# Kernel tuning notes

Measured on AMD Instinct MI355X. Metric: run time of the kernel, lower is better.

## Reference

```python
import jax, jax.numpy as jnp
from jax import lax
import numpy as np

EPS = 1e-5  # torch BatchNorm2d default eps


def _conv_bn_relu_pool(x, w, b, g, beta):
    # Conv2d(k=3, pad=1) -> BatchNorm2d (training mode: batch stats, biased var)
    # -> ReLU -> MaxPool2d(2). x: (N, Cin, H, W), w: (Cout, Cin, 3, 3)
    y = lax.conv_general_dilated(x, w, window_strides=(1, 1), padding='SAME',
                                 dimension_numbers=('NCHW', 'OIHW', 'NCHW'))
    y = y + b[None, :, None, None]
    m = y.mean(axis=(0, 2, 3), keepdims=True)
    v = y.var(axis=(0, 2, 3), keepdims=True)  # biased, matches torch normalization
    y = (y - m) * lax.rsqrt(v + EPS)
    y = y * g[None, :, None, None] + beta[None, :, None, None]
    y = jax.nn.relu(y)
    return lax.reduce_window(y, -jnp.inf, lax.max, (1, 1, 2, 2), (1, 1, 2, 2), 'VALID')


def setup_inputs() -> dict:
    key = jax.random.key(0)
    ks = jax.random.split(key, 20)
    B, T, C, H, W = 16, 64, 3, 32, 32
    F_in = 64 * (H // 4) * (W // 4)  # 4096 flattened CNN features per frame
    n = lambda i, shape, s=0.05: jax.random.normal(ks[i], shape, jnp.float32) * s
    return {
        'x_1': jax.random.normal(ks[0], (B, T, C, H, W), jnp.float32),
        'x_2': jax.random.normal(ks[1], (B, T, C, H, W), jnp.float32),
        'conv1_w': n(2, (64, 2 * C, 3, 3)), 'conv1_b': n(3, (64,)),
        'bn1_g': 1.0 + n(4, (64,)), 'bn1_b': n(5, (64,)),
        'conv2_w': n(6, (64, 64, 3, 3)), 'conv2_b': n(7, (64,)),
        'bn2_g': 1.0 + n(8, (64,)), 'bn2_b': n(9, (64,)),
        'R_w': n(10, (100, 400)), 'R_b': n(11, (100,)),
        'Q_w': n(12, (100, F_in + 100)), 'Q_b': n(13, (100,)),
        'O_w': n(14, (128, 400)), 'O_b': n(15, (128,)),
        'fc1_w': n(16, (64, 128)), 'fc1_b': n(17, (64,)),
        'fc2_w': n(18, (1, 64)), 'fc2_b': n(19, (1,)),
    }


def reference(x_1, x_2, conv1_w, conv1_b, bn1_g, bn1_b, conv2_w, conv2_b,
              bn2_g, bn2_b, R_w, R_b, Q_w, Q_b, O_w, O_b,
              fc1_w, fc1_b, fc2_w, fc2_b):
    B, T = x_1.shape[0], x_1.shape[1]
    x = jnp.concatenate([x_1, x_2], axis=2)            # (B, T, 2C, H, W)
    xr = x.reshape((B * T,) + x.shape[2:])             # fold time into batch
    y = _conv_bn_relu_pool(xr, conv1_w, conv1_b, bn1_g, bn1_b)
    y = _conv_bn_relu_pool(y, conv2_w, conv2_b, bn2_g, bn2_b)
    feats = y.reshape(B, T, -1)                        # (B, T, 4096)

    A = jnp.array([0.0, 0.25, 0.5, 0.95], jnp.float32)  # leaky-integrator decays
    Q_SIZE = 100

    def step(Ha, in_t):
        # Ha: (B, 4, 100); in_t: (B, F_in)
        Hf = Ha.reshape(B, -1)                          # (B, 400) = H_Size
        Rt = jnp.tanh(Hf @ R_w.T + R_b)                 # (B, 100)
        Qt = jnp.tanh(jnp.concatenate([in_t, Rt], axis=1) @ Q_w.T + Q_b)  # (B,100)
        Ha_new = A[None, :, None] * Ha + (1.0 - A)[None, :, None] * Qt[:, None, :]
        return Ha_new, None

    Ha0 = jnp.zeros((B, len(A), Q_SIZE), jnp.float32)
    Ha_T, _ = lax.scan(step, Ha0, jnp.swapaxes(feats, 0, 1))  # scan over T

    # only the last-timestep RNN output feeds the head (out[:, -1, :])
    out_last = jnp.tanh(Ha_T.reshape(B, -1) @ O_w.T + O_b)    # (B, 128)
    h = jax.nn.relu(out_last @ fc1_w.T + fc1_b)               # (B, 64)
    return jax.nn.sigmoid(h @ fc2_w.T + fc2_b)                # (B, 1)
```

## Files before the change

### kernel.cpp

```cpp
#include <hip/hip_runtime.h>
#include <math.h>


typedef __attribute__((ext_vector_type(8))) short s8v;
typedef __attribute__((ext_vector_type(4))) float f32x4;

__device__ __forceinline__ unsigned short f2bf(float f) {
  union { float f; unsigned u; } x; x.f = f;
  return (unsigned short)((x.u + 0x7FFFu + ((x.u >> 16) & 1u)) >> 16);
}
__device__ __forceinline__ float bf2f(unsigned short u) {
  union { unsigned u; float f; } x; x.u = ((unsigned)u) << 16; return x.f;
}
__device__ __forceinline__ float ftanh(float x) {
  float e = __expf(2.f * x);
  return 1.f - 2.f * __builtin_amdgcn_rcpf(e + 1.f);
}

__global__ __launch_bounds__(256)
void w1_pack(const float* __restrict__ w1, unsigned short* __restrict__ wB1)
{
  int i = blockIdx.x*256 + threadIdx.x;
  if (i < 6144) {
    int kh = i >> 11, rem = i & 2047, co = rem >> 5, k2 = rem & 31;
    unsigned short v = 0;
    if (k2 < 18) {
      int kw = k2 / 6, ci = k2 - 6*kw;
      v = f2bf(w1[co*54 + ci*9 + kh*3 + kw]);
    }
    wB1[i] = v;
  }
}

__global__ __launch_bounds__(256, 4)
void conv1_mfma(const float* __restrict__ x1, const float* __restrict__ x2,
                const unsigned short* __restrict__ wB1,
                float* __restrict__ part,
                unsigned short* __restrict__ pmax1, unsigned short* __restrict__ pmin1)
{
  __shared__ unsigned xin[3688];
  __shared__ float wred[4][4][16][2];
  const int n = blockIdx.x, tid = threadIdx.x;
  const int w = tid >> 6, lane = tid & 63;
  const int q = lane >> 4, r = lane & 15;

  s8v bf[3][4];
  #pragma unroll
  for (int kh = 0; kh < 3; ++kh)
    #pragma unroll
    for (int t = 0; t < 4; ++t)
      bf[kh][t] = *(const s8v*)&wB1[kh*2048 + (((t<<4)+r)<<5) + (q<<3)];

  #pragma unroll
  for (int k = 0; k < 15; ++k) {
    int i = tid + (k<<8);
    if (i < 3688) xin[i] = 0;
  }
  __syncthreads();
  #pragma unroll
  for (int k = 0; k < 12; ++k) {
    int i = tid + (k<<8);
    int cp = i >> 10, p = i & 1023;
    int y = p >> 5, x = p & 31;
    float lo, hi;
    if (cp == 0)      { lo = x1[n*3072 + p];        hi = x1[n*3072 + 1024 + p]; }
    else if (cp == 1) { lo = x1[n*3072 + 2048 + p]; hi = x2[n*3072 + p];        }
    else              { lo = x2[n*3072 + 1024 + p]; hi = x2[n*3072 + 2048 + p]; }
    xin[(y+1)*108 + (x+1)*3 + cp] = (unsigned)f2bf(lo) | ((unsigned)f2bf(hi) << 16);
  }
  __syncthreads();

  float st[4], sq[4];
  #pragma unroll
  for (int t = 0; t < 4; ++t) { st[t] = 0.f; sq[t] = 0.f; }
  float pmx[4][2], pmn[4][2];

  #pragma unroll 1
  for (int xb = 0; xb < 2; ++xb) {
    const int xbase = xb << 4;
    #pragma unroll 2
    for (int j = 0; j < 8; ++j) {
      const int y = (w << 3) + j;
      f32x4 acc[4];
      #pragma unroll
      for (int t = 0; t < 4; ++t) acc[t] = (f32x4){0.f,0.f,0.f,0.f};
      #pragma unroll
      for (int kh = 0; kh < 3; ++kh) {
        int dw = (y + kh)*108 + 3*(xbase + r) + (q << 2);
        union { unsigned u[4]; s8v v; } af;
        af.u[0] = xin[dw];   af.u[1] = xin[dw+1];
        af.u[2] = xin[dw+2]; af.u[3] = xin[dw+3];
        #pragma unroll
        for (int t = 0; t < 4; ++t)
          acc[t] = __builtin_amdgcn_mfma_f32_16x16x32_bf16(af.v, bf[kh][t], acc[t], 0, 0, 0);
      }
      #pragma unroll
      for (int t = 0; t < 4; ++t) {
        st[t] += acc[t][0]+acc[t][1]+acc[t][2]+acc[t][3];
        sq[t] = fmaf(acc[t][0],acc[t][0], fmaf(acc[t][1],acc[t][1],
                fmaf(acc[t][2],acc[t][2], fmaf(acc[t][3],acc[t][3], sq[t]))));
      }
      if ((j & 1) == 0) {
        #pragma unroll
        for (int t = 0; t < 4; ++t) {
          pmx[t][0] = fmaxf(acc[t][0], acc[t][1]); pmx[t][1] = fmaxf(acc[t][2], acc[t][3]);
          pmn[t][0] = fminf(acc[t][0], acc[t][1]); pmn[t][1] = fminf(acc[t][2], acc[t][3]);
        }
      } else {
        const int py = y >> 1;
        #pragma unroll
        for (int t = 0; t < 4; ++t) {
          int co = (t << 4) + r;
          #pragma unroll
          for (int pp = 0; pp < 2; ++pp) {
            float mx = fmaxf(pmx[t][pp], fmaxf(acc[t][2*pp], acc[t][2*pp+1]));
            float mn = fminf(pmn[t][pp], fminf(acc[t][2*pp], acc[t][2*pp+1]));
            int pxp = (xb << 3) + (q << 1) + pp;
            int o = (((n << 8) + (py << 4) + pxp) << 6) + co;
            pmax1[o] = f2bf(mx);
            pmin1[o] = f2bf(mn);
          }
        }
      }
    }
  }

  #pragma unroll
  for (int t = 0; t < 4; ++t) {
    float s = st[t], ss = sq[t];
    s  += __shfl_xor(s, 16);  s  += __shfl_xor(s, 32);
    ss += __shfl_xor(ss, 16); ss += __shfl_xor(ss, 32);
    if (q == 0) { wred[w][t][r][0] = s; wred[w][t][r][1] = ss; }
  }
  __syncthreads();
  if (tid < 64) {
    float s = 0.f, ss = 0.f;
    #pragma unroll
    for (int wv = 0; wv < 4; ++wv) {
      s  += wred[wv][tid >> 4][tid & 15][0];
      ss += wred[wv][tid >> 4][tid & 15][1];
    }
    part[tid*2048 + n*2]     = s;
    part[tid*2048 + n*2 + 1] = ss;
  }
}

__global__ __launch_bounds__(256)
void bn_finalize(const float* __restrict__ part, const float* __restrict__ g,
                 const float* __restrict__ beta, float inv_cnt, float* __restrict__ bn)
{
  __shared__ float red[8];
  const int c = blockIdx.x, tid = threadIdx.x;
  float s = 0.f, ss = 0.f;
  for (int n = tid; n < 1024; n += 256) {
    s  += part[c*2048 + n*2];
    ss += part[c*2048 + n*2 + 1];
  }
  #pragma unroll
  for (int d = 32; d; d >>= 1) { s += __shfl_xor(s, d); ss += __shfl_xor(ss, d); }
  if ((tid & 63) == 0) { red[(tid>>6)*2] = s; red[(tid>>6)*2+1] = ss; }
  __syncthreads();
  if (tid == 0) {
    float S  = red[0]+red[2]+red[4]+red[6];
    float SS = red[1]+red[3]+red[5]+red[7];
    float m  = S * inv_cnt;
    float var = SS * inv_cnt - m*m;
    float sc = g[c] * rsqrtf(var + 1e-5f);
    bn[c]    = sc;
    bn[64+c] = beta[c] - m*sc;
  }
}

__global__ __launch_bounds__(256)
void w2_pack(const float* __restrict__ w2, unsigned short* __restrict__ wB)
{
  int i = blockIdx.x*256 + threadIdx.x;
  if (i < 36864) {
    int khw = i >> 12, rem = i & 4095, co = rem >> 6, ci = rem & 63;
    int chunk = (ci >> 3) ^ (co & 7);
    wB[khw*4096 + co*64 + chunk*8 + (ci & 7)] = f2bf(w2[co*576 + ci*9 + khw]);
  }
}

__global__ __launch_bounds__(256)
void qw_pack(const float* __restrict__ Qw, unsigned short* __restrict__ qB)
{
  int i = blockIdx.x*256 + threadIdx.x;
  if (i < 458752) {
    int j = i >> 12, k = i & 4095;
    qB[i] = (j < 100) ? f2bf(Qw[j*4196 + k]) : (unsigned short)0;
  }
}

__global__ __launch_bounds__(256)
void conv2_mfma(const unsigned short* __restrict__ pmax1,
                const unsigned short* __restrict__ pmin1,
                const float* __restrict__ bn1,
                const unsigned short* __restrict__ wB,
                float* __restrict__ part,
                unsigned short* __restrict__ pmax2, unsigned short* __restrict__ pmin2)
{
  __shared__ unsigned short xin[324*64];
  __shared__ unsigned short wL[9*64*64];
  __shared__ float wred[4][4][16][2];
  __shared__ float bnL[128];
  const int n = blockIdx.x, tid = threadIdx.x;
  const int w = tid >> 6, lane = tid & 63;
  const int q = lane >> 4, col = lane & 15;

  if (tid < 128) bnL[tid] = bn1[tid];
  {
    const s8v* src = (const s8v*)wB;
    s8v* dst = (s8v*)wL;
    #pragma unroll
    for (int i = 0; i < 18; ++i) dst[tid + (i<<8)] = src[tid + (i<<8)];
  }
  __syncthreads();
  {
    #pragma unroll
    for (int k = 0; k < 11; ++k) {
      int i = tid + (k<<8);
      if (i < 324*8) {
        int L = i >> 3, s = i & 7;
        int y = L / 18, x = L - y*18;
        s8v v = (s8v){0,0,0,0,0,0,0,0};
        if (y >= 1 && y <= 16 && x >= 1 && x <= 16) {
          int idx = (((n<<8) + ((y-1)<<4) + (x-1))<<6) + (s<<3);
          s8v mx = *(const s8v*)&pmax1[idx];
          s8v mn = *(const s8v*)&pmin1[idx];
          #pragma unroll
          for (int e = 0; e < 8; ++e) {
            int ci = (s<<3) + e;
            float sc = bnL[ci], sh = bnL[64+ci];
            float vv = bf2f((unsigned short)(sc >= 0.f ? mx[e] : mn[e]));
            v[e] = (short)f2bf(fmaxf(fmaf(vv, sc, sh), 0.f));
          }
        }
        *(s8v*)((char*)xin + L*128 + (((s ^ (L & 7)) << 4))) = v;
      }
    }
  }
  __syncthreads();

  f32x4 acc[4][4];
  #pragma unroll
  for (int mt = 0; mt < 4; ++mt)
    #pragma unroll
    for (int t = 0; t < 4; ++t)
      acc[mt][t] = (f32x4){0.f,0.f,0.f,0.f};

  const int py0 = w << 2;
  #pragma unroll 1
  for (int khw = 0; khw < 9; ++khw) {
    const int kh = khw / 3, kw = khw - 3*kh;
    const char* wslice = (const char*)wL + khw*8192;
    #pragma unroll
    for (int ks = 0; ks < 2; ++ks) {
      const int chunk = (ks << 2) + q;
      s8v bfrag[4];
      #pragma unroll
      for (int t = 0; t < 4; ++t) {
        int co = (t << 4) + col;
        bfrag[t] = *(const s8v*)(wslice + co*128 + (((chunk ^ (co & 7)) << 4)));
      }
      #pragma unroll
      for (int mt = 0; mt < 4; ++mt) {
        int L = (py0 + mt + kh)*18 + (col + kw);
        s8v afrag = *(const s8v*)((const char*)xin + L*128 + (((chunk ^ (L & 7)) << 4)));
        #pragma unroll
        for (int t = 0; t < 4; ++t)
          acc[mt][t] = __builtin_amdgcn_mfma_f32_16x16x32_bf16(afrag, bfrag[t], acc[mt][t], 0, 0, 0);
      }
    }
  }

  #pragma unroll
  for (int t = 0; t < 4; ++t) {
    float s = 0.f, ss = 0.f;
    #pragma unroll
    for (int mt = 0; mt < 4; ++mt)
      #pragma unroll
      for (int r = 0; r < 4; ++r) {
        float v = acc[mt][t][r];
        s += v; ss = fmaf(v, v, ss);
      }
    s  += __shfl_xor(s, 16);  s  += __shfl_xor(s, 32);
    ss += __shfl_xor(ss, 16); ss += __shfl_xor(ss, 32);
    if (q == 0) { wred[w][t][col][0] = s; wred[w][t][col][1] = ss; }
  }
  __syncthreads();
  if (tid < 64) {
    float s = 0.f, ss = 0.f;
    #pragma unroll
    for (int wv = 0; wv < 4; ++wv) {
      s  += wred[wv][tid >> 4][tid & 15][0];
      ss += wred[wv][tid >> 4][tid & 15][1];
    }
    part[tid*2048 + n*2]     = s;
    part[tid*2048 + n*2 + 1] = ss;
  }

  #pragma unroll
  for (int t = 0; t < 4; ++t) {
    int co = (t << 4) + col;
    #pragma unroll
    for (int mp = 0; mp < 2; ++mp) {
      f32x4 a0 = acc[2*mp][t], a1 = acc[2*mp+1][t];
      float mx0 = fmaxf(fmaxf(a0[0], a0[1]), fmaxf(a1[0], a1[1]));
      float mx1 = fmaxf(fmaxf(a0[2], a0[3]), fmaxf(a1[2], a1[3]));
      float mn0 = fminf(fminf(a0[0], a0[1]), fminf(a1[0], a1[1]));
      float mn1 = fminf(fminf(a0[2], a0[3]), fminf(a1[2], a1[3]));
      int pyp = (w << 1) + mp;
      int base = ((n*64 + co) << 6) + (pyp << 3) + (q << 1);
      pmax2[base] = f2bf(mx0); pmax2[base+1] = f2bf(mx1);
      pmin2[base] = f2bf(mn0); pmin2[base+1] = f2bf(mn1);
    }
  }
}

__global__ __launch_bounds__(256)
void preq_mfma(const unsigned short* __restrict__ pmax2,
               const unsigned short* __restrict__ pmin2,
               const float* __restrict__ bn2,
               const unsigned short* __restrict__ qB,
               float* __restrict__ part)
{
  const int mb = blockIdx.x, ks = blockIdx.y, tid = threadIdx.x;
  const int w = tid >> 6, lane = tid & 63;
  const int q = lane >> 4, col = lane & 15;
  const int m = (mb << 6) + (w << 4) + col;
  const int k00 = ks << 8;

  f32x4 acc[7];
  #pragma unroll
  for (int t = 0; t < 7; ++t) acc[t] = (f32x4){0.f,0.f,0.f,0.f};

  #pragma unroll 2
  for (int kk = 0; kk < 8; ++kk) {
    const int k = k00 + (kk << 5) + (q << 3);
    const int c = k >> 6;
    const float sc = bn2[c], sh = bn2[64 + c];
    s8v mx = *(const s8v*)&pmax2[m*4096 + k];
    s8v mn = *(const s8v*)&pmin2[m*4096 + k];
    s8v a;
    #pragma unroll
    for (int e = 0; e < 8; ++e) {
      float vv = bf2f((unsigned short)(sc >= 0.f ? mx[e] : mn[e]));
      a[e] = (short)f2bf(fmaxf(fmaf(vv, sc, sh), 0.f));
    }
    #pragma unroll
    for (int t = 0; t < 7; ++t) {
      s8v b = *(const s8v*)&qB[(((t << 4) + col) << 12) + k];
      acc[t] = __builtin_amdgcn_mfma_f32_16x16x32_bf16(a, b, acc[t], 0, 0, 0);
    }
  }

  float* dst = part + ks*114688 + ((mb << 6) + (w << 4) + (q << 2))*112;
  #pragma unroll
  for (int t = 0; t < 7; ++t)
    #pragma unroll
    for (int r = 0; r < 4; ++r)
      dst[r*112 + (t << 4) + col] = acc[t][r];
}

__global__ __launch_bounds__(256)
void preq_reduce(const float* __restrict__ part, const float* __restrict__ Qb,
                 float* __restrict__ preQ)
{
  int idx = blockIdx.x*256 + threadIdx.x;
  if (idx < 1024*100) {
    int n = idx / 100, j = idx - n*100;
    float s = Qb[j];
    #pragma unroll
    for (int ks = 0; ks < 16; ++ks) s += part[ks*114688 + n*112 + j];
    preQ[idx] = s;
  }
}

__global__ __launch_bounds__(512, 2)
void rnn_head(const float* __restrict__ preQ, const float* __restrict__ Rw,
              const float* __restrict__ Rb, const float* __restrict__ Qw,
              const float* __restrict__ Ow, const float* __restrict__ Ob,
              const float* __restrict__ f1w, const float* __restrict__ f1b,
              const float* __restrict__ f2w, const float* __restrict__ f2b,
              float* __restrict__ out)
{
  __shared__ __align__(16) float ha[400];
  __shared__ __align__(16) float rtP[112];
  __shared__ float pq[6400];
  __shared__ float rb[100];
  __shared__ __align__(16) float ol[128];
  __shared__ float f1[64];
  const int b = blockIdx.x, tid = threadIdx.x;

  for (int i = tid; i < 6400; i += 512) pq[i] = preQ[b*6400 + i];
  if (tid < 100) rb[tid] = Rb[tid];
  if (tid < 400) ha[tid] = 0.f;
  if (tid < 112) rtP[tid] = 0.f;

  const int o = tid >> 2, q4 = tid & 3;
  const int rtSlot = (o / 25)*28 + (o % 25);
  float rw[100], qw[28];
  if (tid < 400) {
    const float* rsrc = &Rw[o*400 + q4*100];
    #pragma unroll
    for (int i = 0; i < 25; ++i) {
      float4 v = *(const float4*)&rsrc[i*4];
      rw[i*4] = v.x; rw[i*4+1] = v.y; rw[i*4+2] = v.z; rw[i*4+3] = v.w;
    }
    const float* qsrc = &Qw[o*4196 + 4096 + q4*25];
    #pragma unroll
    for (int i = 0; i < 25; ++i) qw[i] = qsrc[i];
    qw[25] = 0.f; qw[26] = 0.f; qw[27] = 0.f;
  }
  const float Aa = (q4==0) ? 0.f : (q4==1) ? 0.25f : (q4==2) ? 0.5f : 0.95f;
  const float Ba = 1.f - Aa;
  float haReg = 0.f;
  __syncthreads();

  for (int t = 0; t < 64; ++t) {
    if (tid < 400) {
      float r0 = 0.f, r1 = 0.f, r2 = 0.f, r3 = 0.f;
      const float* hp = &ha[q4*100];
      #pragma unroll
      for (int i = 0; i < 25; i += 4) {
        float4 a0 = *(const float4*)&hp[i*4];
        float4 a1 = *(const float4*)&hp[i*4+4];
        float4 a2 = *(const float4*)&hp[i*4+8];
        float4 a3 = *(const float4*)&hp[i*4+12];
        r0 = fmaf(rw[i*4],    a0.x, r0); r0 = fmaf(rw[i*4+1],  a0.y, r0);
        r0 = fmaf(rw[i*4+2],  a0.z, r0); r0 = fmaf(rw[i*4+3],  a0.w, r0);
        if (i+1 < 25) {
          r1 = fmaf(rw[i*4+4],  a1.x, r1); r1 = fmaf(rw[i*4+5],  a1.y, r1);
          r1 = fmaf(rw[i*4+6],  a1.z, r1); r1 = fmaf(rw[i*4+7],  a1.w, r1);
        }
        if (i+2 < 25) {
          r2 = fmaf(rw[i*4+8],  a2.x, r2); r2 = fmaf(rw[i*4+9],  a2.y, r2);
          r2 = fmaf(rw[i*4+10], a2.z, r2); r2 = fmaf(rw[i*4+11], a2.w, r2);
        }
        if (i+3 < 25) {
          r3 = fmaf(rw[i*4+12], a3.x, r3); r3 = fmaf(rw[i*4+13], a3.y, r3);
          r3 = fmaf(rw[i*4+14], a3.z, r3); r3 = fmaf(rw[i*4+15], a3.w, r3);
        }
      }
      float racc = (r0 + r1) + (r2 + r3);
      racc += __shfl_xor(racc, 1);
      racc += __shfl_xor(racc, 2);
      if (q4 == 0) rtP[rtSlot] = ftanh(racc + rb[o]);
    }
    __syncthreads();
    if (tid < 400) {
      float s0 = 0.f, s1 = 0.f;
      const float* rp = &rtP[q4*28];
      #pragma unroll
      for (int i = 0; i < 7; i += 2) {
        float4 v0 = *(const float4*)&rp[i*4];
        s0 = fmaf(qw[i*4],   v0.x, s0); s0 = fmaf(qw[i*4+1], v0.y, s0);
        s0 = fmaf(qw[i*4+2], v0.z, s0); s0 = fmaf(qw[i*4+3], v0.w, s0);
        if (i+1 < 7) {
          float4 v1 = *(const float4*)&rp[i*4+4];
          s1 = fmaf(qw[i*4+4], v1.x, s1); s1 = fmaf(qw[i*4+5], v1.y, s1);
          s1 = fmaf(qw[i*4+6], v1.z, s1); s1 = fmaf(qw[i*4+7], v1.w, s1);
        }
      }
      float qacc = s0 + s1;
      qacc += __shfl_xor(qacc, 1);
      qacc += __shfl_xor(qacc, 2);
      float qt = ftanh(qacc + pq[t*100 + o]);
      haReg = fmaf(Aa, haReg, Ba*qt);
      ha[q4*100 + o] = haReg;
    }
    __syncthreads();
  }

  if (tid < 256) {
    const int j2 = tid >> 1, hh = tid & 1;
    const float* osrc = &Ow[j2*400 + hh*200];
    const float* hp = &ha[hh*200];
    float oacc = 0.f;
    #pragma unroll
    for (int i = 0; i < 50; ++i) {
      float4 w4 = *(const float4*)&osrc[i*4];
      float4 h4 = *(const float4*)&hp[i*4];
      oacc = fmaf(w4.x, h4.x, oacc); oacc = fmaf(w4.y, h4.y, oacc);
      oacc = fmaf(w4.z, h4.z, oacc); oacc = fmaf(w4.w, h4.w, oacc);
    }
    oacc += __shfl_xor(oacc, 1);
    if (hh == 0) ol[j2] = ftanh(oacc + Ob[j2]);
  }
  __syncthreads();
  if (tid < 64) {
    float a = 0.f;
    #pragma unroll
    for (int i = 0; i < 32; ++i) {
      float4 w4 = *(const float4*)&f1w[tid*128 + i*4];
      float4 o4 = *(const float4*)&ol[i*4];
      a = fmaf(w4.x, o4.x, a); a = fmaf(w4.y, o4.y, a);
      a = fmaf(w4.z, o4.z, a); a = fmaf(w4.w, o4.w, a);
    }
    f1[tid] = fmaxf(a + f1b[tid], 0.f);
  }
  __syncthreads();
  if (tid == 0) {
    float a = 0.f;
    for (int i = 0; i < 64; ++i) a = fmaf(f2w[i], f1[i], a);
    out[b] = __builtin_amdgcn_rcpf(1.f + __expf(-a));
  }
}

extern "C" void kernel_launch(void* const* d_in, const int* in_sizes, int n_in,
                              void* d_out, int out_size, void* d_ws, size_t ws_size,
                              hipStream_t stream) {
  (void)in_sizes; (void)n_in; (void)out_size; (void)ws_size;
  const float* x1   = (const float*)d_in[0];
  const float* x2   = (const float*)d_in[1];
  const float* c1w  = (const float*)d_in[2];
  const float* bn1g = (const float*)d_in[4];
  const float* bn1b = (const float*)d_in[5];
  const float* c2w  = (const float*)d_in[6];
  const float* bn2g = (const float*)d_in[8];
  const float* bn2b = (const float*)d_in[9];
  const float* Rw   = (const float*)d_in[10];
  const float* Rb   = (const float*)d_in[11];
  const float* Qw   = (const float*)d_in[12];
  const float* Qb   = (const float*)d_in[13];
  const float* Ow   = (const float*)d_in[14];
  const float* Ob   = (const float*)d_in[15];
  const float* f1w  = (const float*)d_in[16];
  const float* f1b  = (const float*)d_in[17];
  const float* f2w  = (const float*)d_in[18];
  const float* f2b  = (const float*)d_in[19];
  float* outp = (float*)d_out;

  char* wsb = (char*)d_ws;
  unsigned short* pmax1 = (unsigned short*)wsb;
  unsigned short* pmin1 = (unsigned short*)(wsb + 33554432);
  unsigned short* pmax2 = (unsigned short*)(wsb + 67108864);
  unsigned short* pmin2 = (unsigned short*)(wsb + 75497472);
  float* part1  = (float*)(wsb + 83886080);
  float* part2  = part1 + 131072;
  float* bn1    = part2 + 131072;
  float* bn2    = bn1 + 128;
  float* preQ   = bn2 + 128;
  unsigned short* wB1 = (unsigned short*)(preQ + 102400);
  unsigned short* wB2 = wB1 + 6144;
  unsigned short* qB  = wB2 + 36864;
  float* pqpart = (float*)(qB + 458752);

  w1_pack<<<24, 256, 0, stream>>>(c1w, wB1);
  w2_pack<<<144, 256, 0, stream>>>(c2w, wB2);
  qw_pack<<<1792, 256, 0, stream>>>(Qw, qB);
  conv1_mfma<<<1024, 256, 0, stream>>>(x1, x2, wB1, part1, pmax1, pmin1);
  bn_finalize<<<64, 256, 0, stream>>>(part1, bn1g, bn1b, 1.f/1048576.f, bn1);
  conv2_mfma<<<1024, 256, 0, stream>>>(pmax1, pmin1, bn1, wB2, part2, pmax2, pmin2);
  bn_finalize<<<64, 256, 0, stream>>>(part2, bn2g, bn2b, 1.f/262144.f, bn2);
  preq_mfma<<<dim3(16,16), 256, 0, stream>>>(pmax2, pmin2, bn2, qB, pqpart);
  preq_reduce<<<400, 256, 0, stream>>>(pqpart, Qb, preQ);
  rnn_head<<<16, 512, 0, stream>>>(preQ, Rw, Rb, Qw, Ow, Ob, f1w, f1b, f2w, f2b, outp);
}
```

Measured before the change: 186.6 us.

## Store only sign-selected pooled extremum using gamma sign, merge weight pack kernels

```diff
diff --git a/kernel.cpp b/kernel.cpp
--- a/kernel.cpp
+++ b/kernel.cpp
@@ -18,7 +18,10 @@
 }
 
 __global__ __launch_bounds__(256)
-void w1_pack(const float* __restrict__ w1, unsigned short* __restrict__ wB1)
+void pack_all(const float* __restrict__ w1, const float* __restrict__ w2,
+              const float* __restrict__ Qw,
+              unsigned short* __restrict__ wB1, unsigned short* __restrict__ wB2,
+              unsigned short* __restrict__ qB)
 {
   int i = blockIdx.x*256 + threadIdx.x;
   if (i < 6144) {
@@ -29,20 +32,32 @@
       v = f2bf(w1[co*54 + ci*9 + kh*3 + kw]);
     }
     wB1[i] = v;
+  } else if (i < 43008) {
+    int j = i - 6144;
+    int khw = j >> 12, rem = j & 4095, co = rem >> 6, ci = rem & 63;
+    int chunk = (ci >> 3) ^ (co & 7);
+    wB2[khw*4096 + co*64 + chunk*8 + (ci & 7)] = f2bf(w2[co*576 + ci*9 + khw]);
+  } else if (i < 501760) {
+    int j = i - 43008;
+    int row = j >> 12, k = j & 4095;
+    qB[j] = (row < 100) ? f2bf(Qw[row*4196 + k]) : (unsigned short)0;
   }
 }
 
 __global__ __launch_bounds__(256, 4)
 void conv1_mfma(const float* __restrict__ x1, const float* __restrict__ x2,
                 const unsigned short* __restrict__ wB1,
-                float* __restrict__ part,
-                unsigned short* __restrict__ pmax1, unsigned short* __restrict__ pmin1)
+                const float* __restrict__ bn1g,
+                float* __restrict__ part, unsigned short* __restrict__ pool1s)
 {
   __shared__ unsigned xin[3688];
   __shared__ float wred[4][4][16][2];
+  __shared__ float gsel[64];
   const int n = blockIdx.x, tid = threadIdx.x;
   const int w = tid >> 6, lane = tid & 63;
   const int q = lane >> 4, r = lane & 15;
+
+  if (tid < 64) gsel[tid] = bn1g[tid];
 
   s8v bf[3][4];
   #pragma unroll
@@ -111,14 +126,14 @@
         #pragma unroll
         for (int t = 0; t < 4; ++t) {
           int co = (t << 4) + r;
+          const bool useMax = (gsel[co] >= 0.f);
           #pragma unroll
           for (int pp = 0; pp < 2; ++pp) {
             float mx = fmaxf(pmx[t][pp], fmaxf(acc[t][2*pp], acc[t][2*pp+1]));
             float mn = fminf(pmn[t][pp], fminf(acc[t][2*pp], acc[t][2*pp+1]));
             int pxp = (xb << 3) + (q << 1) + pp;
             int o = (((n << 8) + (py << 4) + pxp) << 6) + co;
-            pmax1[o] = f2bf(mx);
-            pmin1[o] = f2bf(mn);
+            pool1s[o] = f2bf(useMax ? mx : mn);
           }
         }
       }
@@ -172,43 +187,23 @@
 }
 
 __global__ __launch_bounds__(256)
-void w2_pack(const float* __restrict__ w2, unsigned short* __restrict__ wB)
-{
-  int i = blockIdx.x*256 + threadIdx.x;
-  if (i < 36864) {
-    int khw = i >> 12, rem = i & 4095, co = rem >> 6, ci = rem & 63;
-    int chunk = (ci >> 3) ^ (co & 7);
-    wB[khw*4096 + co*64 + chunk*8 + (ci & 7)] = f2bf(w2[co*576 + ci*9 + khw]);
-  }
-}
-
-__global__ __launch_bounds__(256)
-void qw_pack(const float* __restrict__ Qw, unsigned short* __restrict__ qB)
-{
-  int i = blockIdx.x*256 + threadIdx.x;
-  if (i < 458752) {
-    int j = i >> 12, k = i & 4095;
-    qB[i] = (j < 100) ? f2bf(Qw[j*4196 + k]) : (unsigned short)0;
-  }
-}
-
-__global__ __launch_bounds__(256)
-void conv2_mfma(const unsigned short* __restrict__ pmax1,
-                const unsigned short* __restrict__ pmin1,
+void conv2_mfma(const unsigned short* __restrict__ pool1s,
                 const float* __restrict__ bn1,
+                const float* __restrict__ bn2g,
                 const unsigned short* __restrict__ wB,
-                float* __restrict__ part,
-                unsigned short* __restrict__ pmax2, unsigned short* __restrict__ pmin2)
+                float* __restrict__ part, unsigned short* __restrict__ psel2)
 {
   __shared__ unsigned short xin[324*64];
   __shared__ unsigned short wL[9*64*64];
   __shared__ float wred[4][4][16][2];
   __shared__ float bnL[128];
+  __shared__ float g2L[64];
   const int n = blockIdx.x, tid = threadIdx.x;
   const int w = tid >> 6, lane = tid & 63;
   const int q = lane >> 4, col = lane & 15;
 
   if (tid < 128) bnL[tid] = bn1[tid];
+  if (tid >= 128 && tid < 192) g2L[tid - 128] = bn2g[tid - 128];
   {
     const s8v* src = (const s8v*)wB;
     s8v* dst = (s8v*)wL;
@@ -226,13 +221,12 @@
         s8v v = (s8v){0,0,0,0,0,0,0,0};
         if (y >= 1 && y <= 16 && x >= 1 && x <= 16) {
           int idx = (((n<<8) + ((y-1)<<4) + (x-1))<<6) + (s<<3);
-          s8v mx = *(const s8v*)&pmax1[idx];
-          s8v mn = *(const s8v*)&pmin1[idx];
+          s8v sv = *(const s8v*)&pool1s[idx];
           #pragma unroll
           for (int e = 0; e < 8; ++e) {
             int ci = (s<<3) + e;
             float sc = bnL[ci], sh = bnL[64+ci];
-            float vv = bf2f((unsigned short)(sc >= 0.f ? mx[e] : mn[e]));
+            float vv = bf2f((unsigned short)sv[e]);
             v[e] = (short)f2bf(fmaxf(fmaf(vv, sc, sh), 0.f));
           }
         }
@@ -303,24 +297,27 @@
   #pragma unroll
   for (int t = 0; t < 4; ++t) {
     int co = (t << 4) + col;
+    const bool useMax = (g2L[co] >= 0.f);
     #pragma unroll
     for (int mp = 0; mp < 2; ++mp) {
       f32x4 a0 = acc[2*mp][t], a1 = acc[2*mp+1][t];
-      float mx0 = fmaxf(fmaxf(a0[0], a0[1]), fmaxf(a1[0], a1[1]));
-      float mx1 = fmaxf(fmaxf(a0[2], a0[3]), fmaxf(a1[2], a1[3]));
-      float mn0 = fminf(fminf(a0[0], a0[1]), fminf(a1[0], a1[1]));
-      float mn1 = fminf(fminf(a0[2], a0[3]), fminf(a1[2], a1[3]));
+      float v0, v1;
+      if (useMax) {
+        v0 = fmaxf(fmaxf(a0[0], a0[1]), fmaxf(a1[0], a1[1]));
+        v1 = fmaxf(fmaxf(a0[2], a0[3]), fmaxf(a1[2], a1[3]));
+      } else {
+        v0 = fminf(fminf(a0[0], a0[1]), fminf(a1[0], a1[1]));
+        v1 = fminf(fminf(a0[2], a0[3]), fminf(a1[2], a1[3]));
+      }
       int pyp = (w << 1) + mp;
       int base = ((n*64 + co) << 6) + (pyp << 3) + (q << 1);
-      pmax2[base] = f2bf(mx0); pmax2[base+1] = f2bf(mx1);
-      pmin2[base] = f2bf(mn0); pmin2[base+1] = f2bf(mn1);
+      psel2[base] = f2bf(v0); psel2[base+1] = f2bf(v1);
     }
   }
 }
 
 __global__ __launch_bounds__(256)
-void preq_mfma(const unsigned short* __restrict__ pmax2,
-               const unsigned short* __restrict__ pmin2,
+void preq_mfma(const unsigned short* __restrict__ psel2,
                const float* __restrict__ bn2,
                const unsigned short* __restrict__ qB,
                float* __restrict__ part)
@@ -340,18 +337,15 @@
     const int k = k00 + (kk << 5) + (q << 3);
     const int c = k >> 6;
     const float sc = bn2[c], sh = bn2[64 + c];
-    s8v mx = *(const s8v*)&pmax2[m*4096 + k];
-    s8v mn = *(const s8v*)&pmin2[m*4096 + k];
+    s8v sv = *(const s8v*)&psel2[m*4096 + k];
     s8v a;
     #pragma unroll
-    for (int e = 0; e < 8; ++e) {
-      float vv = bf2f((unsigned short)(sc >= 0.f ? mx[e] : mn[e]));
-      a[e] = (short)f2bf(fmaxf(fmaf(vv, sc, sh), 0.f));
-    }
+    for (int e = 0; e < 8; ++e)
+      a[e] = (short)f2bf(fmaxf(fmaf(bf2f((unsigned short)sv[e]), sc, sh), 0.f));
     #pragma unroll
     for (int t = 0; t < 7; ++t) {
-      s8v b = *(const s8v*)&qB[(((t << 4) + col) << 12) + k];
-      acc[t] = __builtin_amdgcn_mfma_f32_16x16x32_bf16(a, b, acc[t], 0, 0, 0);
+      s8v bb = *(const s8v*)&qB[(((t << 4) + col) << 12) + k];
+      acc[t] = __builtin_amdgcn_mfma_f32_16x16x32_bf16(a, bb, acc[t], 0, 0, 0);
     }
   }
 
@@ -533,11 +527,9 @@
   float* outp = (float*)d_out;
 
   char* wsb = (char*)d_ws;
-  unsigned short* pmax1 = (unsigned short*)wsb;
-  unsigned short* pmin1 = (unsigned short*)(wsb + 33554432);
-  unsigned short* pmax2 = (unsigned short*)(wsb + 67108864);
-  unsigned short* pmin2 = (unsigned short*)(wsb + 75497472);
-  float* part1  = (float*)(wsb + 83886080);
+  unsigned short* pool1s = (unsigned short*)wsb;
+  unsigned short* psel2  = (unsigned short*)(wsb + 33554432);
+  float* part1  = (float*)(wsb + 41943040);
   float* part2  = part1 + 131072;
   float* bn1    = part2 + 131072;
   float* bn2    = bn1 + 128;
@@ -547,14 +539,12 @@
   unsigned short* qB  = wB2 + 36864;
   float* pqpart = (float*)(qB + 458752);
 
-  w1_pack<<<24, 256, 0, stream>>>(c1w, wB1);
-  w2_pack<<<144, 256, 0, stream>>>(c2w, wB2);
-  qw_pack<<<1792, 256, 0, stream>>>(Qw, qB);
-  conv1_mfma<<<1024, 256, 0, stream>>>(x1, x2, wB1, part1, pmax1, pmin1);
+  pack_all<<<1960, 256, 0, stream>>>(c1w, c2w, Qw, wB1, wB2, qB);
+  conv1_mfma<<<1024, 256, 0, stream>>>(x1, x2, wB1, bn1g, part1, pool1s);
   bn_finalize<<<64, 256, 0, stream>>>(part1, bn1g, bn1b, 1.f/1048576.f, bn1);
-  conv2_mfma<<<1024, 256, 0, stream>>>(pmax1, pmin1, bn1, wB2, part2, pmax2, pmin2);
+  conv2_mfma<<<1024, 256, 0, stream>>>(pool1s, bn1, bn2g, wB2, part2, psel2);
   bn_finalize<<<64, 256, 0, stream>>>(part2, bn2g, bn2b, 1.f/262144.f, bn2);
-  preq_mfma<<<dim3(16,16), 256, 0, stream>>>(pmax2, pmin2, bn2, qB, pqpart);
+  preq_mfma<<<dim3(16,16), 256, 0, stream>>>(psel2, bn2, qB, pqpart);
   preq_reduce<<<400, 256, 0, stream>>>(pqpart, Qb, preQ);
   rnn_head<<<16, 512, 0, stream>>>(preQ, Rw, Rb, Qw, Ow, Ob, f1w, f1b, f2w, f2b, outp);
 }
```

Result: faster. 172.4 us (median of 2 runs) (-7.6%).
